# Kernel tuning notes

Hardware: AMD Instinct MI355X
Metric: run time of the kernel (lower is better)

## Reference

```python
import math
import jax, jax.numpy as jnp
from jax import lax
import numpy as np

B, S, D = 64, 257, 768
H, HD = 12, 64  # heads, head_dim; D == H*HD


def setup_inputs() -> dict:
    key = jax.random.key(0)
    ks = jax.random.split(key, 12)
    sc = 0.02
    return {
        "hidden_states": jax.random.normal(ks[0], (B, S, D), jnp.float32),
        "Wq": jax.random.normal(ks[1], (D, D), jnp.float32) * sc,
        "bq": jax.random.normal(ks[2], (D,), jnp.float32) * sc,
        "Wk": jax.random.normal(ks[3], (D, D), jnp.float32) * sc,
        "bk": jax.random.normal(ks[4], (D,), jnp.float32) * sc,
        "Wv": jax.random.normal(ks[5], (D, D), jnp.float32) * sc,
        "bv": jax.random.normal(ks[6], (D,), jnp.float32) * sc,
        "Wo": jax.random.normal(ks[7], (D, D), jnp.float32) * sc,
        "bo": jax.random.normal(ks[8], (D,), jnp.float32) * sc,
        "conv1_w": jax.random.normal(ks[9], (D, 1, 1, 1), jnp.float32) * sc,
        "conv2_w": jax.random.normal(ks[10], (D, 1, 3, 3), jnp.float32) * sc,
        "conv3_w": jax.random.normal(ks[11], (D, 1, 5, 5), jnp.float32) * sc,
    }


def reference(hidden_states, Wq, bq, Wk, bk, Wv, bv, Wo, bo, conv1_w, conv2_w, conv3_w):
    scale = 1.0 / math.sqrt(HD)
    # Q over full sequence (cls + 256 patches)
    q = (hidden_states @ Wq.T + bq).reshape(B, S, H, HD).transpose(0, 2, 1, 3)  # [B,H,S,HD]
    cls_tok = hidden_states[:, :1]                                   # [B,1,D]
    x = hidden_states[:, 1:].transpose(0, 2, 1).reshape(B, D, 16, 16)  # NCHW
    ctx = jnp.zeros((B, H, S, HD), hidden_states.dtype)
    for cw in (conv1_w, conv2_w, conv3_w):  # depthwise convs, VALID padding
        xb = lax.conv_general_dilated(x, cw, (1, 1), 'VALID',
                                      feature_group_count=D)         # [B,D,h,w]
        xb = xb.reshape(B, D, -1).transpose(0, 2, 1)                  # [B,L-1,D]
        xb = jnp.concatenate([cls_tok, xb], axis=1)                   # [B,L,D]
        L = xb.shape[1]
        k = (xb @ Wk.T + bk).reshape(B, L, H, HD).transpose(0, 2, 1, 3)
        v = (xb @ Wv.T + bv).reshape(B, L, H, HD).transpose(0, 2, 1, 3)
        scores = jnp.einsum('bhqd,bhkd->bhqk', q, k) * scale
        probs = jax.nn.softmax(scores, axis=-1)
        ctx = ctx + jnp.einsum('bhqk,bhkd->bhqd', probs, v)
    ctx = (ctx / 3.0).transpose(0, 2, 1, 3).reshape(B, S, D)
    return ctx @ Wo.T + bo
```

## Files before the change

kernel.cpp:

```cpp
#include <hip/hip_runtime.h>

using bf16   = __bf16;
using bf16x4 = __bf16 __attribute__((ext_vector_type(4)));
using bf16x8 = __bf16 __attribute__((ext_vector_type(8)));
using f32x4  = float __attribute__((ext_vector_type(4)));

#define MFMA_BF16(a, b, c) __builtin_amdgcn_mfma_f32_16x16x32_bf16((a), (b), (c), 0, 0, 0)

constexpr int BATCH = 64, SEQ = 257, DIM = 768, NH = 12;
constexpr size_t WE = (size_t)DIM * DIM;

__device__ inline void gload_lds16(const bf16* g, bf16* l) {
  __builtin_amdgcn_global_load_lds(
      (const __attribute__((address_space(1))) void*)g,
      (__attribute__((address_space(3))) void*)l, 16, 0, 0);
}

__global__ __launch_bounds__(256) void cvt_weights6(
    const float* __restrict__ wq, const float* __restrict__ wk,
    const float* __restrict__ wv, const float* __restrict__ wo,
    const float* __restrict__ c1, bf16* __restrict__ dst) {
  const size_t i = (size_t)blockIdx.x * 256 + threadIdx.x;
  const size_t per = WE / 4;
  if (i >= 6 * per) return;
  const int region = (int)(i / per);
  const size_t within = i % per;
  const float* srcs[6] = {wq, wk, wv, wk, wv, wo};
  const float4 f = ((const float4*)srcs[region])[within];
  float v[4] = {f.x, f.y, f.z, f.w};
  if (region == 1 || region == 2) {
    const int c0 = (int)((within * 4) % DIM);
#pragma unroll
    for (int j = 0; j < 4; ++j) v[j] *= c1[c0 + j];
  }
  bf16* o = dst + i * 4;
#pragma unroll
  for (int j = 0; j < 4; ++j) o[j] = (bf16)v[j];
}

__global__ __launch_bounds__(256) void cvt_hs(const float* __restrict__ src,
                                              bf16* __restrict__ dst, int n4) {
  const int i = blockIdx.x * 256 + threadIdx.x;
  if (i >= n4) return;
  const float4 f = ((const float4*)src)[i];
  bf16* o = dst + (size_t)i * 4;
  o[0] = (bf16)f.x; o[1] = (bf16)f.y; o[2] = (bf16)f.z; o[3] = (bf16)f.w;
}

template <int KS>
__global__ __launch_bounds__(256) void conv_kernel(
    const float* __restrict__ hs, const float* __restrict__ cw, bf16* __restrict__ xb) {
  constexpr int OW = 17 - KS;
  constexpr int NOUT = OW * OW;
  constexpr int L = NOUT + 1;
  constexpr int KSQ = KS * KS;
  constexpr int NP = (NOUT + 7) / 8;
  __shared__ float hsl[256][36];
  __shared__ float wsm[32][KSQ];

  const int t = threadIdx.x;
  const int b = blockIdx.y;
  const int c0 = blockIdx.x * 32;

  const float* src = hs + ((size_t)b * SEQ + 1 + t) * DIM + c0;
#pragma unroll
  for (int j = 0; j < 8; ++j) *(float4*)&hsl[t][4 * j] = ((const float4*)src)[j];

  if (t < 32) {
#pragma unroll
    for (int q = 0; q < KSQ; ++q) wsm[t][q] = cw[(size_t)(c0 + t) * KSQ + q];
    const float cv = hs[(size_t)b * SEQ * DIM + c0 + t];
    xb[(size_t)b * L * DIM + c0 + t] = (bf16)cv;
  }
  __syncthreads();

  const int c = t & 31, pg = t >> 5;
#pragma unroll
  for (int i = 0; i < NP; ++i) {
    const int p = pg * NP + i;
    if (p < NOUT) {
      const int oi = p / OW, oj = p - oi * OW;
      float a = 0.f;
#pragma unroll
      for (int di = 0; di < KS; ++di)
#pragma unroll
        for (int dj = 0; dj < KS; ++dj)
          a += hsl[(oi + di) * 16 + oj + dj][c] * wsm[c][di * KS + dj];
      xb[((size_t)b * L + 1 + p) * DIM + c0 + c] = (bf16)a;
    }
  }
}

template <int OUT>
__device__ __forceinline__ void gemm_core(
    bf16* sm, const bf16* A, const bf16* W,
    const float* b0, const float* b1, const float* b2,
    void* Y0, void* Y1, void* Y2, int M, int L, int Lv, int tM, int tN, int tid) {
  constexpr int BUF_E = 128 * 32;
  bf16* smA = sm;
  bf16* smB = sm + 3 * BUF_E;

  const int lane = tid & 63;
  const int w = tid >> 6;
  const int wr = (w >> 1) * 64, wc = (w & 1) * 64;
  const int rl = lane & 15;
  const int g = lane >> 4;
  const int kqs = ((g ^ ((rl >> 1) & 3)) << 3);

  const int sr = lane >> 2;
  const int sk = (((lane & 3) ^ ((sr >> 1) & 3)) << 3);
  const int r0 = w * 32 + sr;
  const int r1 = w * 32 + 16 + sr;
  long ga0 = (long)tM * 128 + r0; if (ga0 >= M) ga0 = M - 1;
  long ga1 = (long)tM * 128 + r1; if (ga1 >= M) ga1 = M - 1;
  const bf16* pa0 = A + ga0 * DIM + sk;
  const bf16* pa1 = A + ga1 * DIM + sk;
  const bf16* pb0 = W + ((size_t)tN * 128 + r0) * DIM + sk;
  const bf16* pb1 = W + ((size_t)tN * 128 + r1) * DIM + sk;
  const int lbase = (w * 32) * 32;

  const f32x4 zero4 = {0.f, 0.f, 0.f, 0.f};
  f32x4 acc[4][4];
#pragma unroll
  for (int m = 0; m < 4; ++m)
#pragma unroll
    for (int n = 0; n < 4; ++n) acc[m][n] = zero4;

  constexpr int NT = DIM / 32;

#define STAGE(kt_, buf_)                                      \
  do {                                                        \
    const int kb_ = (kt_) * 32;                               \
    bf16* a_ = smA + (buf_) * BUF_E + lbase;                  \
    bf16* b_ = smB + (buf_) * BUF_E + lbase;                  \
    gload_lds16(pa0 + kb_, a_);                               \
    gload_lds16(pa1 + kb_, a_ + 512);                         \
    gload_lds16(pb0 + kb_, b_);                               \
    gload_lds16(pb1 + kb_, b_ + 512);                         \
  } while (0)

  STAGE(0, 0);
  STAGE(1, 1);
  asm volatile("s_waitcnt vmcnt(4)" ::: "memory");
  __builtin_amdgcn_s_barrier();
  __builtin_amdgcn_sched_barrier(0);

  int buf = 0;
  for (int kt = 0; kt < NT; ++kt) {
    const bf16* Ac = smA + buf * BUF_E;
    const bf16* Bc = smB + buf * BUF_E;
    bf16x8 af[4], bfr[4];
#pragma unroll
    for (int m = 0; m < 4; ++m) af[m] = *(const bf16x8*)&Ac[(wr + m * 16 + rl) * 32 + kqs];
#pragma unroll
    for (int n = 0; n < 4; ++n) bfr[n] = *(const bf16x8*)&Bc[(wc + n * 16 + rl) * 32 + kqs];
#pragma unroll
    for (int m = 0; m < 4; ++m)
#pragma unroll
      for (int n = 0; n < 4; ++n) acc[m][n] = MFMA_BF16(af[m], bfr[n], acc[m][n]);

    if (kt + 2 < NT) {
      const int nb = buf + 2 >= 3 ? buf - 1 : buf + 2;
      STAGE(kt + 2, nb);
    }
    if (kt + 1 < NT) {
      if (kt + 2 < NT) asm volatile("s_waitcnt vmcnt(4)" ::: "memory");
      else             asm volatile("s_waitcnt vmcnt(0)" ::: "memory");
      __builtin_amdgcn_s_barrier();
      __builtin_amdgcn_sched_barrier(0);
    }
    buf = buf == 2 ? 0 : buf + 1;
  }
#undef STAGE

  if constexpr (OUT == 3) {
#pragma unroll
    for (int n = 0; n < 4; ++n) {
      const int gcol = tN * 128 + wc + n * 16 + rl;
      const float bia = b0[gcol];
#pragma unroll
      for (int m = 0; m < 4; ++m) {
#pragma unroll
        for (int i = 0; i < 4; ++i) {
          const long grow = (long)tM * 128 + wr + m * 16 + g * 4 + i;
          if (grow < M) ((float*)Y0)[grow * DIM + gcol] = acc[m][n][i] + bia;
        }
      }
    }
    return;
  }

  constexpr int TP = 136;
  bf16* smT = sm;
  __syncthreads();

  const bool vpath = (OUT == 1 && tN >= 6) || (OUT == 4 && tN >= 12);
  const bool qpath = (OUT == 4 && tN < 6);

  if (vpath) {
    const int cbase = (OUT == 4) ? 1536 : 768;
    const float* bv_ = (OUT == 4) ? b2 : b1;
#pragma unroll
    for (int n = 0; n < 4; ++n) {
      const int col = wc + n * 16 + rl;
      const float bia = bv_[tN * 128 + col - cbase];
#pragma unroll
      for (int m = 0; m < 4; ++m) {
        const int row = wr + m * 16 + g * 4;
        bf16x4 v4;
#pragma unroll
        for (int i = 0; i < 4; ++i) v4[i] = (bf16)(acc[m][n][i] + bia);
        *(bf16x4*)(smT + col * TP + row) = v4;
      }
    }
    __syncthreads();
    bf16* vout = (bf16*)((OUT == 4) ? Y2 : Y1);
    const int tNv = tN - ((OUT == 4) ? 12 : 6);
#pragma unroll
    for (int it = 0; it < 8; ++it) {
      const int c = it * 256 + tid;
      const int coll = c >> 4;
      const int rw0 = (c & 15) * 8;
      const long g2 = (long)tM * 128 + rw0;
      if (g2 < M) {
        const int b2i = (int)(g2 / L);
        const int l2 = (int)(g2 - (long)b2i * L);
        const int cv = tNv * 128 + coll;
        bf16* dst = vout + (((size_t)b2i * NH + (cv >> 6)) * 64 + (cv & 63)) * Lv;
        const bf16x8 v = *(const bf16x8*)(smT + coll * TP + rw0);
        if (l2 + 8 <= L) {
          *(bf16x8*)(dst + l2) = v;
        } else {
#pragma unroll
          for (int j = 0; j < 8; ++j) {
            const long g3 = g2 + j;
            const int b3 = (int)(g3 / L), l3 = (int)(g3 - (long)b3 * L);
            vout[(((size_t)b3 * NH + (cv >> 6)) * 64 + (cv & 63)) * Lv + l3] = v[j];
          }
        }
      }
    }
  } else {
    const float scale = qpath ? 0.125f : 1.f;
#pragma unroll
    for (int n = 0; n < 4; ++n) {
      const int col = wc + n * 16 + rl;
      const int gcol = tN * 128 + col;
      float bia;
      if constexpr (OUT == 4) bia = (gcol < 768) ? b0[gcol] : b1[gcol - 768];
      else                    bia = b0[gcol];
#pragma unroll
      for (int m = 0; m < 4; ++m) {
#pragma unroll
        for (int i = 0; i < 4; ++i) {
          const int row = wr + m * 16 + g * 4 + i;
          smT[row * TP + col] = (bf16)((acc[m][n][i] + bia) * scale);
        }
      }
    }
    __syncthreads();
    bf16* kout = (bf16*)((OUT == 4 && !qpath) ? Y1 : Y0);
    const int coff = (OUT == 4 && !qpath) ? 768 : 0;
    const bool kswz = !qpath;
#pragma unroll
    for (int it = 0; it < 8; ++it) {
      const int c = it * 256 + tid;
      const int row = c >> 4;
      const int col0 = (c & 15) * 8;
      const long g2 = (long)tM * 128 + row;
      if (g2 < M) {
        const int b2i = (int)(g2 / L);
        const int l2 = (int)(g2 - (long)b2i * L);
        const int gc = tN * 128 + col0 - coff;
        const bf16x8 v = *(const bf16x8*)(smT + row * TP + col0);
        int dchunk = (gc & 63) >> 3;
        if (kswz) dchunk ^= (l2 & 7);
        *(bf16x8*)(kout + (((size_t)b2i * NH + (gc >> 6)) * L + l2) * 64 + dchunk * 8) = v;
      }
    }
  }
}

__device__ __forceinline__ int m204_swz(int orig, int nwg) {
  const int nq = nwg >> 3, rr = nwg & 7, xcd = orig & 7, base = orig >> 3;
  return (xcd < rr ? xcd * (nq + 1) : rr * (nq + 1) + (xcd - rr) * nq) + base;
}

__global__ __launch_bounds__(256, 4) void gemm_qkv0_kernel(
    const bf16* __restrict__ A, const bf16* __restrict__ W,
    const float* __restrict__ bq, const float* __restrict__ bk, const float* __restrict__ bv,
    bf16* __restrict__ qb, bf16* __restrict__ kb, bf16* __restrict__ vb) {
  constexpr int BUF_E = 128 * 32;
  __shared__ alignas(16) bf16 sm[6 * BUF_E];
  const int wgid = m204_swz(blockIdx.x, gridDim.x);
  const int tM = wgid / 18, tN = wgid - tM * 18;
  gemm_core<4>(sm, A, W, bq, bk, bv, qb, kb, vb, BATCH * SEQ, 257, 264, tM, tN, threadIdx.x);
}

__global__ __launch_bounds__(256, 4) void gemm_kv12_kernel(
    const bf16* __restrict__ A1, const bf16* __restrict__ A2, const bf16* __restrict__ W,
    const float* __restrict__ bk, const float* __restrict__ bv,
    bf16* __restrict__ k1, bf16* __restrict__ v1,
    bf16* __restrict__ k2, bf16* __restrict__ v2) {
  constexpr int BUF_E = 128 * 32;
  __shared__ alignas(16) bf16 sm[6 * BUF_E];
  const int wgid = m204_swz(blockIdx.x, gridDim.x);
  if (wgid < 1188) {
    const int tM = wgid / 12, tN = wgid - tM * 12;
    gemm_core<1>(sm, A1, W, bk, bv, nullptr, k1, v1, nullptr, BATCH * 197, 197, 200, tM, tN, threadIdx.x);
  } else {
    const int l = wgid - 1188;
    const int tM = l / 12, tN = l - tM * 12;
    gemm_core<1>(sm, A2, W, bk, bv, nullptr, k2, v2, nullptr, BATCH * 145, 145, 152, tM, tN, threadIdx.x);
  }
}

__global__ __launch_bounds__(256, 4) void gemm_o_kernel(
    const bf16* __restrict__ A, const bf16* __restrict__ W,
    const float* __restrict__ bo, float* __restrict__ out) {
  constexpr int BUF_E = 128 * 32;
  __shared__ alignas(16) bf16 sm[6 * BUF_E];
  const int wgid = m204_swz(blockIdx.x, gridDim.x);
  const int tM = wgid / 6, tN = wgid - tM * 6;
  gemm_core<3>(sm, A, W, bo, nullptr, nullptr, out, nullptr, nullptr, BATCH * SEQ, 257, 1, tM, tN, threadIdx.x);
}

__global__ __launch_bounds__(256) void cls_fixup_kernel(
    const bf16* __restrict__ hsb, const bf16* __restrict__ wk, const bf16* __restrict__ wv,
    const float* __restrict__ bk, const float* __restrict__ bv,
    bf16* __restrict__ k12, bf16* __restrict__ v12) {
  __shared__ float hrow[DIM];
  const int b = blockIdx.y, tile = blockIdx.x, t = threadIdx.x;
  for (int i = t; i < DIM; i += 256) hrow[i] = (float)hsb[(size_t)b * SEQ * DIM + i];
  __syncthreads();
  const bool isv = tile >= 6;
  const int o = (tile - (isv ? 6 : 0)) * 128 + (t >> 1);
  const int half = t & 1;
  const bf16* wrow = (isv ? wv : wk) + (size_t)o * DIM + half * 384;
  float s = 0.f;
#pragma unroll 4
  for (int k = 0; k < 48; ++k) {
    const bf16x8 wv8 = *(const bf16x8*)(wrow + k * 8);
#pragma unroll
    for (int j = 0; j < 8; ++j) s += hrow[half * 384 + k * 8 + j] * (float)wv8[j];
  }
  s += __shfl_xor(s, 1);
  if (!half) {
    s += (isv ? bv : bk)[o];
    if (!isv) {
      k12[(((size_t)b * NH + (o >> 6)) * 257) * 64 + (o & 63)] = (bf16)s;
    } else {
      v12[(((size_t)b * NH + (o >> 6)) * 64 + (o & 63)) * 264] = (bf16)s;
    }
  }
}

template <int L, int BRANCH>
__global__ __launch_bounds__(256, 2) void attn_kernel(
    const bf16* __restrict__ qb, const bf16* __restrict__ kb, const bf16* __restrict__ vb,
    float* __restrict__ ctx, bf16* __restrict__ xbuf, int Lv) {
  constexpr int LK16 = (L + 15) & ~15;
  constexpr int NKT = LK16 / 16;
  constexpr int LP32 = (L + 31) & ~31;
  constexpr int NK32 = LP32 / 32;
  constexpr int PSTR = LP32 + 8;
  __shared__ alignas(16) bf16 Ks[LK16 * 64];
  __shared__ alignas(16) bf16 Ps[64 * PSTR];

  const int tid = threadIdx.x, lane = tid & 63, w = tid >> 6;
  const int orig = blockIdx.x;
  const int nper = gridDim.x >> 3;
  const int bh = (orig & 7) * nper + (orig >> 3);
  const int b = bh / NH, h = bh % NH;
  const int cl = lane & 15, g = lane >> 4;

  const bf16* kbase = kb + (size_t)bh * L * 64;
  for (int c = tid; c < LK16 * 8; c += 256)
    gload_lds16(kbase + (size_t)c * 8, Ks + (size_t)c * 8);
  __syncthreads();

  const bf16* vbase = vb + (size_t)bh * 64 * Lv;

  for (int qt = 0; qt < 5; ++qt) {
    int sq = qt * 64 + w * 16 + cl;
    if (sq > 256) sq = 256;
    const bf16* qrow = qb + ((size_t)bh * 257 + sq) * 64 + g * 8;
    const bf16x8 aq0 = *(const bf16x8*)qrow;
    const bf16x8 aq1 = *(const bf16x8*)(qrow + 32);

    float sums[4] = {0.f, 0.f, 0.f, 0.f};
    const int prow0 = (w * 16 + g * 4) * PSTR + cl;
#pragma unroll
    for (int kt = 0; kt < NKT; ++kt) {
      const int key0 = kt * 16 + cl;
      const int sw = key0 & 7;
      const char* krow = (const char*)Ks + key0 * 128;
      const bf16x8 bk0 = *(const bf16x8*)(krow + ((g ^ sw) << 4));
      const bf16x8 bk1 = *(const bf16x8*)(krow + (((4 + g) ^ sw) << 4));
      f32x4 z = {0.f, 0.f, 0.f, 0.f};
      z = MFMA_BF16(aq0, bk0, z);
      z = MFMA_BF16(aq1, bk1, z);
      const bool valid = key0 < L;
#pragma unroll
      for (int j = 0; j < 4; ++j) {
        const float p = valid ? __expf(z[j]) : 0.f;
        sums[j] += p;
        Ps[prow0 + j * PSTR + kt * 16] = (bf16)p;
      }
    }
    if constexpr (LP32 > LK16) {
#pragma unroll
      for (int j = 0; j < 4; ++j) Ps[prow0 + j * PSTR + LK16] = (bf16)0.f;
    }

    bf16x8 vr0[4], vr1[4];
#pragma unroll
    for (int nt = 0; nt < 4; ++nt)
      vr0[nt] = *(const bf16x8*)(vbase + (size_t)(nt * 16 + cl) * Lv + g * 8);

#pragma unroll
    for (int j = 0; j < 4; ++j) {
      sums[j] += __shfl_xor(sums[j], 1);
      sums[j] += __shfl_xor(sums[j], 2);
      sums[j] += __shfl_xor(sums[j], 4);
      sums[j] += __shfl_xor(sums[j], 8);
    }
    float inv[4];
#pragma unroll
    for (int j = 0; j < 4; ++j) inv[j] = 1.f / sums[j];

    f32x4 cacc[4];
#pragma unroll
    for (int nt = 0; nt < 4; ++nt) cacc[nt] = f32x4{0.f, 0.f, 0.f, 0.f};
#pragma unroll
    for (int kt = 0; kt < NK32; ++kt) {
      const bool even = (kt & 1) == 0;
      if (kt + 1 < NK32) {
        int kk = (kt + 1) * 32 + g * 8;
        if (kk > Lv - 8) kk = Lv - 8;
#pragma unroll
        for (int nt = 0; nt < 4; ++nt) {
          const bf16x8 v = *(const bf16x8*)(vbase + (size_t)(nt * 16 + cl) * Lv + kk);
          if (even) vr1[nt] = v; else vr0[nt] = v;
        }
      }
      const bf16x8 ap = *(const bf16x8*)&Ps[(w * 16 + cl) * PSTR + kt * 32 + g * 8];
#pragma unroll
      for (int nt = 0; nt < 4; ++nt)
        cacc[nt] = MFMA_BF16(ap, even ? vr0[nt] : vr1[nt], cacc[nt]);
    }

#pragma unroll
    for (int nt = 0; nt < 4; ++nt) {
#pragma unroll
      for (int i = 0; i < 4; ++i) {
        const int s_q = qt * 64 + w * 16 + g * 4 + i;
        if (s_q < 257) {
          const size_t idx = ((size_t)b * 257 + s_q) * DIM + h * 64 + nt * 16 + cl;
          const float val = cacc[nt][i] * inv[i];
          if constexpr (BRANCH == 0)
            ctx[idx] = val;
          else if constexpr (BRANCH == 1)
            ctx[idx] += val;
          else
            xbuf[idx] = (bf16)((ctx[idx] + val) * (1.f / 3.f));
        }
      }
    }
  }
}

extern "C" void kernel_launch(void* const* d_in, const int* in_sizes, int n_in,
                              void* d_out, int out_size, void* d_ws, size_t ws_size,
                              hipStream_t stream) {
  (void)in_sizes; (void)n_in; (void)out_size; (void)ws_size;
  const float* hs = (const float*)d_in[0];
  const float* Wq = (const float*)d_in[1];
  const float* bq = (const float*)d_in[2];
  const float* Wk = (const float*)d_in[3];
  const float* bk = (const float*)d_in[4];
  const float* Wv = (const float*)d_in[5];
  const float* bv = (const float*)d_in[6];
  const float* Wo = (const float*)d_in[7];
  const float* bo = (const float*)d_in[8];
  const float* c1 = (const float*)d_in[9];
  const float* c2 = (const float*)d_in[10];
  const float* c3 = (const float*)d_in[11];
  float* out = (float*)d_out;

  constexpr size_t QB = (size_t)BATCH * NH * SEQ * 64;
  constexpr size_t XB = (size_t)BATCH * SEQ * DIM;
  constexpr size_t K12 = (size_t)BATCH * NH * 257 * 64;
  constexpr size_t V12 = (size_t)BATCH * NH * 64 * 264;
  constexpr size_t XB3 = (size_t)BATCH * 145 * DIM;
  constexpr size_t K3 = (size_t)BATCH * NH * 145 * 64;

  bf16* wbf = (bf16*)d_ws;
  bf16* qb  = wbf + 6 * WE;
  bf16* xb  = qb + QB;
  bf16* k12 = xb + XB;
  bf16* v12 = k12 + K12;
  bf16* xb3 = v12 + V12;
  bf16* k3  = xb3 + XB3;
  bf16* v3  = k3 + K3;
  bf16* hsb = xb;

  cvt_weights6<<<dim3((unsigned)((6 * WE / 4 + 255) / 256)), 256, 0, stream>>>(Wq, Wk, Wv, Wo, c1, wbf);
  cvt_hs<<<dim3((BATCH * SEQ * DIM / 4 + 255) / 256), 256, 0, stream>>>(hs, hsb, BATCH * SEQ * DIM / 4);

  gemm_qkv0_kernel<<<dim3(129 * 18), 256, 0, stream>>>(hsb, wbf, bq, bk, bv, qb, k12, v12);
  cls_fixup_kernel<<<dim3(12, 64), 256, 0, stream>>>(hsb, wbf + 3 * WE, wbf + 4 * WE, bk, bv, k12, v12);
  attn_kernel<257, 0><<<dim3(768), 256, 0, stream>>>(qb, k12, v12, out, xb, 264);

  conv_kernel<3><<<dim3(24, 64), 256, 0, stream>>>(hs, c2, xb);
  conv_kernel<5><<<dim3(24, 64), 256, 0, stream>>>(hs, c3, xb3);
  gemm_kv12_kernel<<<dim3(1188 + 876), 256, 0, stream>>>(xb, xb3, wbf + 3 * WE, bk, bv,
                                                         k12, v12, k3, v3);
  attn_kernel<197, 1><<<dim3(768), 256, 0, stream>>>(qb, k12, v12, out, xb, 200);
  attn_kernel<145, 2><<<dim3(768), 256, 0, stream>>>(qb, k3, v3, out, xb, 152);

  gemm_o_kernel<<<dim3(129 * 6), 256, 0, stream>>>(xb, wbf + 5 * WE, bo, out);
}
```

Before: 514.6 us.

## Widen GEMM tiles to 128x256 with 512-thread workgroups

Changes the shared GEMM core from 128x128 tiles run by 4 waves to 128x256 tiles run by 8 waves, with each wave still computing a 64x64 sub-tile. The B tile is loaded by twice as many waves, so each A row block is fetched once per 256 output columns instead of once per 128. The epilogue transpose and scatter paths are rewritten for the wider tile, and grid sizes are halved for the QKV, KV and output GEMMs. This cuts global and LDS traffic for A and the number of workgroups, at the cost of more LDS per block (72 KB), which may lower occupancy.

```diff
diff --git a/kernel.cpp b/kernel.cpp
--- a/kernel.cpp
+++ b/kernel.cpp
@@ -96,28 +96,28 @@
     bf16* sm, const bf16* A, const bf16* W,
     const float* b0, const float* b1, const float* b2,
     void* Y0, void* Y1, void* Y2, int M, int L, int Lv, int tM, int tN, int tid) {
-  constexpr int BUF_E = 128 * 32;
+  constexpr int A_E = 128 * 32;
+  constexpr int B_E = 256 * 32;
   bf16* smA = sm;
-  bf16* smB = sm + 3 * BUF_E;
+  bf16* smB = sm + 3 * A_E;
 
   const int lane = tid & 63;
   const int w = tid >> 6;
-  const int wr = (w >> 1) * 64, wc = (w & 1) * 64;
+  const int wrow = (w >> 2) * 64;
+  const int wcol = (w & 3) * 64;
   const int rl = lane & 15;
   const int g = lane >> 4;
   const int kqs = ((g ^ ((rl >> 1) & 3)) << 3);
 
   const int sr = lane >> 2;
   const int sk = (((lane & 3) ^ ((sr >> 1) & 3)) << 3);
-  const int r0 = w * 32 + sr;
-  const int r1 = w * 32 + 16 + sr;
-  long ga0 = (long)tM * 128 + r0; if (ga0 >= M) ga0 = M - 1;
-  long ga1 = (long)tM * 128 + r1; if (ga1 >= M) ga1 = M - 1;
-  const bf16* pa0 = A + ga0 * DIM + sk;
-  const bf16* pa1 = A + ga1 * DIM + sk;
-  const bf16* pb0 = W + ((size_t)tN * 128 + r0) * DIM + sk;
-  const bf16* pb1 = W + ((size_t)tN * 128 + r1) * DIM + sk;
-  const int lbase = (w * 32) * 32;
+  long gar = (long)tM * 128 + w * 16 + sr; if (gar >= M) gar = M - 1;
+  const bf16* pa  = A + gar * DIM + sk;
+  const bf16* pb0 = W + ((size_t)tN * 256 + (2 * w) * 16 + sr) * DIM + sk;
+  const bf16* pb1 = W + ((size_t)tN * 256 + (2 * w + 1) * 16 + sr) * DIM + sk;
+  const int la  = w * 512;
+  const int lb0 = (2 * w) * 512;
+  const int lb1 = (2 * w + 1) * 512;
 
   const f32x4 zero4 = {0.f, 0.f, 0.f, 0.f};
   f32x4 acc[4][4];
@@ -131,29 +131,26 @@
 #define STAGE(kt_, buf_)                                      \
   do {                                                        \
     const int kb_ = (kt_) * 32;                               \
-    bf16* a_ = smA + (buf_) * BUF_E + lbase;                  \
-    bf16* b_ = smB + (buf_) * BUF_E + lbase;                  \
-    gload_lds16(pa0 + kb_, a_);                               \
-    gload_lds16(pa1 + kb_, a_ + 512);                         \
-    gload_lds16(pb0 + kb_, b_);                               \
-    gload_lds16(pb1 + kb_, b_ + 512);                         \
+    gload_lds16(pa  + kb_, smA + (buf_) * A_E + la);          \
+    gload_lds16(pb0 + kb_, smB + (buf_) * B_E + lb0);         \
+    gload_lds16(pb1 + kb_, smB + (buf_) * B_E + lb1);         \
   } while (0)
 
   STAGE(0, 0);
   STAGE(1, 1);
-  asm volatile("s_waitcnt vmcnt(4)" ::: "memory");
+  asm volatile("s_waitcnt vmcnt(3)" ::: "memory");
   __builtin_amdgcn_s_barrier();
   __builtin_amdgcn_sched_barrier(0);
 
   int buf = 0;
   for (int kt = 0; kt < NT; ++kt) {
-    const bf16* Ac = smA + buf * BUF_E;
-    const bf16* Bc = smB + buf * BUF_E;
+    const bf16* Ac = smA + buf * A_E;
+    const bf16* Bc = smB + buf * B_E;
     bf16x8 af[4], bfr[4];
 #pragma unroll
-    for (int m = 0; m < 4; ++m) af[m] = *(const bf16x8*)&Ac[(wr + m * 16 + rl) * 32 + kqs];
-#pragma unroll
-    for (int n = 0; n < 4; ++n) bfr[n] = *(const bf16x8*)&Bc[(wc + n * 16 + rl) * 32 + kqs];
+    for (int m = 0; m < 4; ++m) af[m] = *(const bf16x8*)&Ac[(wrow + m * 16 + rl) * 32 + kqs];
+#pragma unroll
+    for (int n = 0; n < 4; ++n) bfr[n] = *(const bf16x8*)&Bc[(wcol + n * 16 + rl) * 32 + kqs];
 #pragma unroll
     for (int m = 0; m < 4; ++m)
 #pragma unroll
@@ -164,7 +161,7 @@
       STAGE(kt + 2, nb);
     }
     if (kt + 1 < NT) {
-      if (kt + 2 < NT) asm volatile("s_waitcnt vmcnt(4)" ::: "memory");
+      if (kt + 2 < NT) asm volatile("s_waitcnt vmcnt(3)" ::: "memory");
       else             asm volatile("s_waitcnt vmcnt(0)" ::: "memory");
       __builtin_amdgcn_s_barrier();
       __builtin_amdgcn_sched_barrier(0);
@@ -176,13 +173,13 @@
   if constexpr (OUT == 3) {
 #pragma unroll
     for (int n = 0; n < 4; ++n) {
-      const int gcol = tN * 128 + wc + n * 16 + rl;
+      const int gcol = tN * 256 + wcol + n * 16 + rl;
       const float bia = b0[gcol];
 #pragma unroll
       for (int m = 0; m < 4; ++m) {
 #pragma unroll
         for (int i = 0; i < 4; ++i) {
-          const long grow = (long)tM * 128 + wr + m * 16 + g * 4 + i;
+          const long grow = (long)tM * 128 + wrow + m * 16 + g * 4 + i;
           if (grow < M) ((float*)Y0)[grow * DIM + gcol] = acc[m][n][i] + bia;
         }
       }
@@ -190,44 +187,44 @@
     return;
   }
 
-  constexpr int TP = 136;
   bf16* smT = sm;
   __syncthreads();
 
-  const bool vpath = (OUT == 1 && tN >= 6) || (OUT == 4 && tN >= 12);
-  const bool qpath = (OUT == 4 && tN < 6);
+  const bool qpath = (OUT == 4) && (tN < 3);
+  const bool vpath = (OUT == 4) ? (tN >= 6) : (tN >= 3);
 
   if (vpath) {
+    constexpr int TPV = 136;
     const int cbase = (OUT == 4) ? 1536 : 768;
     const float* bv_ = (OUT == 4) ? b2 : b1;
 #pragma unroll
     for (int n = 0; n < 4; ++n) {
-      const int col = wc + n * 16 + rl;
-      const float bia = bv_[tN * 128 + col - cbase];
+      const int col = wcol + n * 16 + rl;
+      const float bia = bv_[tN * 256 + col - cbase];
 #pragma unroll
       for (int m = 0; m < 4; ++m) {
-        const int row = wr + m * 16 + g * 4;
+        const int row = wrow + m * 16 + g * 4;
         bf16x4 v4;
 #pragma unroll
         for (int i = 0; i < 4; ++i) v4[i] = (bf16)(acc[m][n][i] + bia);
-        *(bf16x4*)(smT + col * TP + row) = v4;
+        *(bf16x4*)(smT + col * TPV + row) = v4;
       }
     }
     __syncthreads();
     bf16* vout = (bf16*)((OUT == 4) ? Y2 : Y1);
-    const int tNv = tN - ((OUT == 4) ? 12 : 6);
+    const int tNv = tN - ((OUT == 4) ? 6 : 3);
 #pragma unroll
     for (int it = 0; it < 8; ++it) {
-      const int c = it * 256 + tid;
+      const int c = it * 512 + tid;
       const int coll = c >> 4;
       const int rw0 = (c & 15) * 8;
       const long g2 = (long)tM * 128 + rw0;
       if (g2 < M) {
         const int b2i = (int)(g2 / L);
         const int l2 = (int)(g2 - (long)b2i * L);
-        const int cv = tNv * 128 + coll;
+        const int cv = tNv * 256 + coll;
         bf16* dst = vout + (((size_t)b2i * NH + (cv >> 6)) * 64 + (cv & 63)) * Lv;
-        const bf16x8 v = *(const bf16x8*)(smT + coll * TP + rw0);
+        const bf16x8 v = *(const bf16x8*)(smT + coll * TPV + rw0);
         if (l2 + 8 <= L) {
           *(bf16x8*)(dst + l2) = v;
         } else {
@@ -241,41 +238,46 @@
       }
     }
   } else {
+    constexpr int TPK = 264;
     const float scale = qpath ? 0.125f : 1.f;
 #pragma unroll
     for (int n = 0; n < 4; ++n) {
-      const int col = wc + n * 16 + rl;
-      const int gcol = tN * 128 + col;
+      const int col = wcol + n * 16 + rl;
+      const int gcol = tN * 256 + col;
       float bia;
-      if constexpr (OUT == 4) bia = (gcol < 768) ? b0[gcol] : b1[gcol - 768];
+      if constexpr (OUT == 4) bia = qpath ? b0[gcol] : b1[gcol - 768];
       else                    bia = b0[gcol];
 #pragma unroll
       for (int m = 0; m < 4; ++m) {
 #pragma unroll
         for (int i = 0; i < 4; ++i) {
-          const int row = wr + m * 16 + g * 4 + i;
-          smT[row * TP + col] = (bf16)((acc[m][n][i] + bia) * scale);
+          const int row = wrow + m * 16 + g * 4 + i;
+          smT[row * TPK + col] = (bf16)((acc[m][n][i] + bia) * scale);
         }
       }
     }
     __syncthreads();
-    bf16* kout = (bf16*)((OUT == 4 && !qpath) ? Y1 : Y0);
+    bf16* kout = (bf16*)(qpath ? Y0 : ((OUT == 4) ? Y1 : Y0));
     const int coff = (OUT == 4 && !qpath) ? 768 : 0;
     const bool kswz = !qpath;
 #pragma unroll
     for (int it = 0; it < 8; ++it) {
-      const int c = it * 256 + tid;
-      const int row = c >> 4;
-      const int col0 = (c & 15) * 8;
+      const int c = it * 512 + tid;
+      const int row = c >> 5;
+      const int col0 = (c & 31) * 8;
       const long g2 = (long)tM * 128 + row;
       if (g2 < M) {
         const int b2i = (int)(g2 / L);
         const int l2 = (int)(g2 - (long)b2i * L);
-        const int gc = tN * 128 + col0 - coff;
-        const bf16x8 v = *(const bf16x8*)(smT + row * TP + col0);
-        int dchunk = (gc & 63) >> 3;
-        if (kswz) dchunk ^= (l2 & 7);
-        *(bf16x8*)(kout + (((size_t)b2i * NH + (gc >> 6)) * L + l2) * 64 + dchunk * 8) = v;
+        const int gc = tN * 256 + col0 - coff;
+        const bf16x8 v = *(const bf16x8*)(smT + row * TPK + col0);
+        if (qpath) {
+          *(bf16x8*)(kout + (((size_t)b2i * NH + (gc >> 6)) * 257 + l2) * 64 + (gc & 63)) = v;
+        } else {
+          int dchunk = (gc & 63) >> 3;
+          if (kswz) dchunk ^= (l2 & 7);
+          *(bf16x8*)(kout + (((size_t)b2i * NH + (gc >> 6)) * L + l2) * 64 + dchunk * 8) = v;
+        }
       }
     }
   }
@@ -286,42 +288,39 @@
   return (xcd < rr ? xcd * (nq + 1) : rr * (nq + 1) + (xcd - rr) * nq) + base;
 }
 
-__global__ __launch_bounds__(256, 4) void gemm_qkv0_kernel(
+__global__ __launch_bounds__(512, 4) void gemm_qkv0_kernel(
     const bf16* __restrict__ A, const bf16* __restrict__ W,
     const float* __restrict__ bq, const float* __restrict__ bk, const float* __restrict__ bv,
     bf16* __restrict__ qb, bf16* __restrict__ kb, bf16* __restrict__ vb) {
-  constexpr int BUF_E = 128 * 32;
-  __shared__ alignas(16) bf16 sm[6 * BUF_E];
+  __shared__ alignas(16) bf16 sm[36864];
   const int wgid = m204_swz(blockIdx.x, gridDim.x);
-  const int tM = wgid / 18, tN = wgid - tM * 18;
+  const int tM = wgid / 9, tN = wgid - tM * 9;
   gemm_core<4>(sm, A, W, bq, bk, bv, qb, kb, vb, BATCH * SEQ, 257, 264, tM, tN, threadIdx.x);
 }
 
-__global__ __launch_bounds__(256, 4) void gemm_kv12_kernel(
+__global__ __launch_bounds__(512, 4) void gemm_kv12_kernel(
     const bf16* __restrict__ A1, const bf16* __restrict__ A2, const bf16* __restrict__ W,
     const float* __restrict__ bk, const float* __restrict__ bv,
     bf16* __restrict__ k1, bf16* __restrict__ v1,
     bf16* __restrict__ k2, bf16* __restrict__ v2) {
-  constexpr int BUF_E = 128 * 32;
-  __shared__ alignas(16) bf16 sm[6 * BUF_E];
+  __shared__ alignas(16) bf16 sm[36864];
   const int wgid = m204_swz(blockIdx.x, gridDim.x);
-  if (wgid < 1188) {
-    const int tM = wgid / 12, tN = wgid - tM * 12;
+  if (wgid < 594) {
+    const int tM = wgid / 6, tN = wgid - tM * 6;
     gemm_core<1>(sm, A1, W, bk, bv, nullptr, k1, v1, nullptr, BATCH * 197, 197, 200, tM, tN, threadIdx.x);
   } else {
-    const int l = wgid - 1188;
-    const int tM = l / 12, tN = l - tM * 12;
+    const int l = wgid - 594;
+    const int tM = l / 6, tN = l - tM * 6;
     gemm_core<1>(sm, A2, W, bk, bv, nullptr, k2, v2, nullptr, BATCH * 145, 145, 152, tM, tN, threadIdx.x);
   }
 }
 
-__global__ __launch_bounds__(256, 4) void gemm_o_kernel(
+__global__ __launch_bounds__(512, 4) void gemm_o_kernel(
     const bf16* __restrict__ A, const bf16* __restrict__ W,
     const float* __restrict__ bo, float* __restrict__ out) {
-  constexpr int BUF_E = 128 * 32;
-  __shared__ alignas(16) bf16 sm[6 * BUF_E];
+  __shared__ alignas(16) bf16 sm[36864];
   const int wgid = m204_swz(blockIdx.x, gridDim.x);
-  const int tM = wgid / 6, tN = wgid - tM * 6;
+  const int tM = wgid / 3, tN = wgid - tM * 3;
   gemm_core<3>(sm, A, W, bo, nullptr, nullptr, out, nullptr, nullptr, BATCH * SEQ, 257, 1, tM, tN, threadIdx.x);
 }
 
@@ -508,16 +507,16 @@
   cvt_weights6<<<dim3((unsigned)((6 * WE / 4 + 255) / 256)), 256, 0, stream>>>(Wq, Wk, Wv, Wo, c1, wbf);
   cvt_hs<<<dim3((BATCH * SEQ * DIM / 4 + 255) / 256), 256, 0, stream>>>(hs, hsb, BATCH * SEQ * DIM / 4);
 
-  gemm_qkv0_kernel<<<dim3(129 * 18), 256, 0, stream>>>(hsb, wbf, bq, bk, bv, qb, k12, v12);
+  gemm_qkv0_kernel<<<dim3(129 * 9), 512, 0, stream>>>(hsb, wbf, bq, bk, bv, qb, k12, v12);
   cls_fixup_kernel<<<dim3(12, 64), 256, 0, stream>>>(hsb, wbf + 3 * WE, wbf + 4 * WE, bk, bv, k12, v12);
   attn_kernel<257, 0><<<dim3(768), 256, 0, stream>>>(qb, k12, v12, out, xb, 264);
 
   conv_kernel<3><<<dim3(24, 64), 256, 0, stream>>>(hs, c2, xb);
   conv_kernel<5><<<dim3(24, 64), 256, 0, stream>>>(hs, c3, xb3);
-  gemm_kv12_kernel<<<dim3(1188 + 876), 256, 0, stream>>>(xb, xb3, wbf + 3 * WE, bk, bv,
-                                                         k12, v12, k3, v3);
+  gemm_kv12_kernel<<<dim3(594 + 438), 512, 0, stream>>>(xb, xb3, wbf + 3 * WE, bk, bv,
+                                                        k12, v12, k3, v3);
   attn_kernel<197, 1><<<dim3(768), 256, 0, stream>>>(qb, k12, v12, out, xb, 200);
   attn_kernel<145, 2><<<dim3(768), 256, 0, stream>>>(qb, k3, v3, out, xb, 152);
 
-  gemm_o_kernel<<<dim3(129 * 6), 256, 0, stream>>>(xb, wbf + 5 * WE, bo, out);
-}
+  gemm_o_kernel<<<dim3(129 * 3), 512, 0, stream>>>(xb, wbf + 5 * WE, bo, out);
+}
```

After: 479.4 us, median of 2. -6.8%, faster.
